# Optimization experiments

Hardware: AMD Instinct MI355X
Metric: run time of the kernel (lower is better)

## Reference

```python
import jax, jax.numpy as jnp
import numpy as np

B, S, V, D, P, HOPS = 512, 512, 50000, 300, 3, 3


def setup_inputs() -> dict:
    rng = np.random.default_rng(0)
    # left-padded text indices (zeros first, tokens last), as implied by locationed_memory
    lens = rng.integers(32, S + 1, size=B)
    txt = np.zeros((B, S), dtype=np.int64)
    for i in range(B):
        txt[i, S - lens[i]:] = rng.integers(1, V, size=lens[i])
    alens = rng.integers(1, 9, size=B)
    asp = np.zeros((B, 8), dtype=np.int64)
    for i in range(B):
        asp[i, :alens[i]] = rng.integers(1, V, size=alens[i])

    key = jax.random.key(0)
    ks = jax.random.split(key, 8)
    emb = jax.random.normal(ks[0], (V, D), dtype=jnp.float32) * 0.1
    emb = emb.at[0].set(0.0)  # padding row
    s = 1.0 / np.sqrt(D)
    Wx = jax.random.uniform(ks[1], (D, D), minval=-s, maxval=s)
    bx = jnp.zeros((D,), jnp.float32)
    Wk = jax.random.uniform(ks[2], (D, D), minval=-s, maxval=s)
    bk = jnp.zeros((D,), jnp.float32)
    Wq = jax.random.uniform(ks[3], (D, D), minval=-s, maxval=s)
    bq = jnp.zeros((D,), jnp.float32)
    w_mlp = jax.random.uniform(ks[4], (2 * D,), minval=-s, maxval=s)
    Wp = jax.random.uniform(ks[5], (D, D), minval=-s, maxval=s)
    bp = jnp.zeros((D,), jnp.float32)
    Wd = jax.random.uniform(ks[6], (P, D), minval=-s, maxval=s)
    bd = jnp.zeros((P,), jnp.float32)
    return {"text_idx": jnp.asarray(txt), "aspect_idx": jnp.asarray(asp),
            "emb": emb, "Wx": Wx, "bx": bx, "Wk": Wk, "bk": bk,
            "Wq": Wq, "bq": bq, "w_mlp": w_mlp, "Wp": Wp, "bp": bp,
            "Wd": Wd, "bd": bd}


def reference(text_idx, aspect_idx, emb, Wx, bx, Wk, bk, Wq, bq, w_mlp, Wp, bp, Wd, bd):
    lens = jnp.sum(text_idx != 0, axis=-1)                      # (B,)
    memory = emb[text_idx]                                       # (B,S,D)
    # vectorized locationed_memory: token j (0-based within the sequence) at
    # position idx = S - len + j gets weight 1 - j/len; padding positions keep 1
    pos = jnp.arange(S)[None, :]                                 # (1,S)
    j = pos - (S - lens)[:, None]                                # (B,S)
    lf = lens[:, None].astype(jnp.float32)
    w = jnp.where(j >= 0, 1.0 - j.astype(jnp.float32) / lf, 1.0)
    memory = memory * w[:, :, None]

    n_asp = jnp.sum(aspect_idx != 0, axis=-1).astype(jnp.float32)  # (B,)
    aspect = jnp.sum(emb[aspect_idx], axis=1) / n_asp[:, None]     # (B,D)

    kx = memory @ Wk.T + bk                                      # (B,S,D) key proj (same every hop)
    wk_part, wq_part = w_mlp[:D], w_mlp[D:]
    k_score = kx @ wk_part                                       # (B,S) precomputed kx contribution

    x = aspect                                                   # (B,D) == squeeze of (B,1,D)
    for _ in range(HOPS):
        x = x @ Wx.T + bx
        qx = x @ Wq.T + bq                                       # (B,D)
        # mlp score: tanh(cat(kx, qx) @ w_mlp) = tanh(kx@w_k + qx@w_q)
        score = jnp.tanh(k_score + (qx @ wq_part)[:, None])      # (B,S)
        attn = jax.nn.softmax(score, axis=-1)                    # (B,S)
        out = jnp.einsum('bs,bsd->bd', attn, kx)                 # (B,D)
        out = out @ Wp.T + bp
        x = out + x
    return x @ Wd.T + bd                                         # (B,P)
```

## Files before the change

### kernel.cpp

```cpp
#include <hip/hip_runtime.h>
#include <hip/hip_fp16.h>

#define DD 300
#define SS 512
#define VV 50000

#define CK       0
#define CQS      1
#define BU       2
#define BW1      3
#define C3A      4
#define C3B      8
#define C3C      12
#define U_OFF    16
#define UQWX_OFF 320
#define W1_OFF   640
#define W2_OFF   960
#define D0_OFF   1280
#define P1_OFF   2240
#define P2_OFF   2560
#define D1_OFF   2880
#define D2_OFF   3840
#define D3_OFF   4800
#define TAB_OFF  8192

#define FMA4(acc, s, v) { acc.x += (s)*(v).x; acc.y += (s)*(v).y; \
                          acc.z += (s)*(v).z; acc.w += (s)*(v).w; }

__device__ __forceinline__ float fast_exp_tanh(float z) {
    const float t = __expf(2.0f * z);
    return __expf(1.0f - 2.0f / (t + 1.0f));
}

__device__ __forceinline__ float wred(float v) {
    #pragma unroll
    for (int off = 32; off; off >>= 1) v += __shfl_xor(v, off);
    return v;
}

__device__ __forceinline__ void vcomb(
    const float* __restrict__ M, const float* __restrict__ sIn,
    float* __restrict__ sOut, float* __restrict__ buf,
    const int tid, const int wv, const int lane)
{
    float4 a0{0,0,0,0}, a1{0,0,0,0};
    for (int e = wv; e < DD; e += 16) {
        const float4* kr = (const float4*)(M + e * DD);
        const float s = sIn[e];
        FMA4(a0, s, kr[lane]);
        if (lane < 11) { const float4 k1 = kr[64 + lane]; FMA4(a1, s, k1); }
    }
    float4* pr = (float4*)(buf + wv * 304);
    pr[lane] = a0;
    if (lane < 11) pr[64 + lane] = a1;
    __syncthreads();
    if (tid < DD) {
        float s = 0.f;
        #pragma unroll
        for (int w = 0; w < 16; ++w) s += buf[w * 304 + tid];
        sOut[tid] = s;
    }
    __syncthreads();
}

__device__ __forceinline__ void rowcomb3(
    const float* __restrict__ M, const float (*sIn)[304], float (*sOut)[304],
    float* __restrict__ buf, const int tid, const int wv, const int lane)
{
    float4 a00{0,0,0,0}, a01{0,0,0,0}, a10{0,0,0,0},
           a11{0,0,0,0}, a20{0,0,0,0}, a21{0,0,0,0};
    for (int e = wv; e < DD; e += 16) {
        const float4* kr = (const float4*)(M + e * DD);
        const float4 k0 = kr[lane];
        const float p0 = sIn[0][e], p1 = sIn[1][e], p2 = sIn[2][e];
        FMA4(a00, p0, k0); FMA4(a10, p1, k0); FMA4(a20, p2, k0);
        if (lane < 11) {
            const float4 k1 = kr[64 + lane];
            FMA4(a01, p0, k1); FMA4(a11, p1, k1); FMA4(a21, p2, k1);
        }
    }
    float4* p0r = (float4*)(buf + (wv * 3 + 0) * 304);
    float4* p1r = (float4*)(buf + (wv * 3 + 1) * 304);
    float4* p2r = (float4*)(buf + (wv * 3 + 2) * 304);
    p0r[lane] = a00; p1r[lane] = a10; p2r[lane] = a20;
    if (lane < 11) { p0r[64+lane] = a01; p1r[64+lane] = a11; p2r[64+lane] = a21; }
    __syncthreads();
    if (tid < DD) {
        #pragma unroll
        for (int r = 0; r < 3; ++r) {
            float s = 0.f;
            for (int w = 0; w < 16; ++w) s += buf[(w * 3 + r) * 304 + tid];
            sOut[r][tid] = s;
        }
    }
    __syncthreads();
}

__device__ __forceinline__ void bpass(
    const float* __restrict__ Wp, const float* __restrict__ bp,
    const float* __restrict__ bx, const float* __restrict__ sbk,
    float* __restrict__ sB, const int wv, const int lane)
{
    const float4* b4 = (const float4*)sbk;
    const float4 k0 = b4[lane];
    const float4 k1 = (lane < 11) ? b4[64 + lane] : float4{0, 0, 0, 0};
    for (int i2 = wv; i2 < DD; i2 += 16) {
        const float4* wr = (const float4*)(Wp + i2 * DD);
        const float4 w0 = wr[lane];
        float a = w0.x * k0.x + w0.y * k0.y + w0.z * k0.z + w0.w * k0.w;
        if (lane < 11) {
            const float4 w1 = wr[64 + lane];
            a += w1.x * k1.x + w1.y * k1.y + w1.z * k1.z + w1.w * k1.w;
        }
        a = wred(a);
        if (lane == 0) sB[i2] = a + bp[i2] + bx[i2];
    }
    __syncthreads();
}

__global__ __launch_bounds__(1024) void pre(
    const float* __restrict__ Wk, const float* __restrict__ bk,
    const float* __restrict__ Wq, const float* __restrict__ bq,
    const float* __restrict__ w_mlp,
    const float* __restrict__ Wp, const float* __restrict__ bp,
    const float* __restrict__ Wx, const float* __restrict__ bx,
    const float* __restrict__ Wd, const float* __restrict__ bd,
    float* __restrict__ ws)
{
    const int blk  = blockIdx.x;
    const int tid  = threadIdx.x;
    const int wv   = tid >> 6;
    const int lane = tid & 63;
    __shared__ __align__(16) float buf[16 * 304 * 3];
    __shared__ __align__(16) float v0[304], v1[304], v2[304], v3[304], v4[304], vB[304];
    __shared__ __align__(16) float m0[3][304], m1[3][304], mW[3][304];

    if (blk == 0) {
        if (tid < DD) v0[tid] = w_mlp[tid];
        __syncthreads();
        vcomb(Wk, v0, v1, buf, tid, wv, lane);
        if (tid < DD) ws[U_OFF + tid] = v1[tid];
        if (wv == 0) {
            float c = 0.f;
            for (int j = lane; j < DD; j += 64) c += v0[j] * bk[j];
            c = wred(c);
            if (lane == 0) ws[CK] = c;
        }
        return;
    }

    if (blk == 1) {
        if (tid < DD) v0[tid] = w_mlp[DD + tid];
        __syncthreads();
        vcomb(Wq, v0, v1, buf, tid, wv, lane);
        vcomb(Wx, v1, v2, buf, tid, wv, lane);
        vcomb(Wx, v2, v3, buf, tid, wv, lane);
        vcomb(Wx, v3, v4, buf, tid, wv, lane);
        if (tid < DD) {
            ws[UQWX_OFF + tid] = v2[tid];
            ws[W1_OFF + tid]   = v3[tid];
            ws[W2_OFF + tid]   = v4[tid];
        }
        if (wv == 0) {
            float c = 0.f;
            for (int j = lane; j < DD; j += 64) c += v0[j] * bq[j] + v1[j] * bx[j];
            c = wred(c);
            if (lane == 0) ws[CQS] = c;
        }
        __syncthreads();
        if (tid < DD) v1[tid] = bk[tid];
        __syncthreads();
        bpass(Wp, bp, bx, v1, vB, wv, lane);
        if (wv == 0) {
            float a = 0.f, b = 0.f;
            for (int j = lane; j < DD; j += 64) { a += vB[j] * v2[j]; b += vB[j] * v3[j]; }
            a = wred(a); b = wred(b);
            if (lane == 0) { ws[BU] = a; ws[BW1] = b; }
        }
        return;
    }

    if (blk == 2 || blk == 3) {
        if (tid < DD) v0[tid] = w_mlp[DD + tid];
        __syncthreads();
        vcomb(Wq, v0, v1, buf, tid, wv, lane);
        vcomb(Wx, v1, v2, buf, tid, wv, lane);
        if (blk == 2) {
            vcomb(Wp, v2, v3, buf, tid, wv, lane);
            vcomb(Wk, v3, v4, buf, tid, wv, lane);
            if (tid < DD) ws[P1_OFF + tid] = v4[tid];
        } else {
            vcomb(Wx, v2, v3, buf, tid, wv, lane);
            vcomb(Wp, v3, v4, buf, tid, wv, lane);
            vcomb(Wk, v4, v0, buf, tid, wv, lane);
            if (tid < DD) ws[P2_OFF + tid] = v0[tid];
        }
        return;
    }

    for (int r = tid; r < 3 * DD; r += 1024) mW[r / DD][r % DD] = Wd[r];
    __syncthreads();

    if (blk == 4) {
        rowcomb3(Wx, mW, m0, buf, tid, wv, lane);
        rowcomb3(Wx, m0, m1, buf, tid, wv, lane);
        if (tid < DD) v1[tid] = bk[tid];
        __syncthreads();
        bpass(Wp, bp, bx, v1, vB, wv, lane);
        if (wv < 3) {
            float ca = 0.f, cb = 0.f, cc = 0.f;
            for (int j = lane; j < DD; j += 64) {
                const float b = vB[j];
                ca += m0[wv][j] * b; cb += m1[wv][j] * b; cc += mW[wv][j] * b;
            }
            ca = wred(ca); cb = wred(cb); cc = wred(cc);
            if (lane == 0) {
                ws[C3A + wv] = ca;
                ws[C3B + wv] = cb;
                ws[C3C + wv] = cc + bd[wv];
            }
        }
        rowcomb3(Wx, m1, m0, buf, tid, wv, lane);
        for (int r = tid; r < 3 * DD; r += 1024) ws[D0_OFF + r] = m0[r / DD][r % DD];
        return;
    }
    if (blk == 5) {
        rowcomb3(Wp, mW, m0, buf, tid, wv, lane);
        rowcomb3(Wk, m0, m1, buf, tid, wv, lane);
        for (int r = tid; r < 3 * DD; r += 1024) ws[D3_OFF + r] = m1[r / DD][r % DD];
        return;
    }
    if (blk == 6) {
        rowcomb3(Wx, mW, m0, buf, tid, wv, lane);
        rowcomb3(Wp, m0, m1, buf, tid, wv, lane);
        rowcomb3(Wk, m1, m0, buf, tid, wv, lane);
        for (int r = tid; r < 3 * DD; r += 1024) ws[D2_OFF + r] = m0[r / DD][r % DD];
        return;
    }
    {
        rowcomb3(Wx, mW, m0, buf, tid, wv, lane);
        rowcomb3(Wx, m0, m1, buf, tid, wv, lane);
        rowcomb3(Wp, m1, m0, buf, tid, wv, lane);
        rowcomb3(Wk, m0, m1, buf, tid, wv, lane);
        for (int r = tid; r < 3 * DD; r += 1024) ws[D1_OFF + r] = m1[r / DD][r % DD];
    }
}

__global__ __launch_bounds__(256) void build_tables(
    const float* __restrict__ emb, const float* __restrict__ wsr,
    float* __restrict__ tab)
{
    const int tid  = threadIdx.x;
    const int lane = tid & 63;
    const int m    = lane & 3;
    const int q    = lane >> 2;

    __shared__ __align__(16) float4 Vl[76 * 12];

    if (tid < 12) Vl[75 * 12 + tid] = float4{0, 0, 0, 0};
#define STAGE_V(k, off) \
    { const float4* src = (const float4*)(wsr + (off)); \
      for (int j = tid; j < 75; j += 256) Vl[j * 12 + (k)] = src[j]; }
    STAGE_V(0,  P1_OFF)
    STAGE_V(1,  P2_OFF)
    STAGE_V(2,  D1_OFF)
    STAGE_V(3,  D1_OFF + DD)
    STAGE_V(4,  D1_OFF + 2 * DD)
    STAGE_V(5,  D2_OFF)
    STAGE_V(6,  D2_OFF + DD)
    STAGE_V(7,  D2_OFF + 2 * DD)
    STAGE_V(8,  D3_OFF)
    STAGE_V(9,  D3_OFF + DD)
    STAGE_V(10, D3_OFF + 2 * DD)
    STAGE_V(11, U_OFF)
#undef STAGE_V
    __syncthreads();

    const int task = blockIdx.x * 4 + (tid >> 6);
    if (task >= VV / 16) return;
    const int row = task * 16 + q;

    const float4* er4 = (const float4*)(emb + (size_t)row * DD);

    float4 e[19];
    #pragma unroll
    for (int t = 0; t < 19; ++t) {
        const int j = m + 4 * t;
        if (j < 75) e[t] = er4[j];
        else        e[t] = float4{0, 0, 0, 0};
    }

    float acc[12];
    #pragma unroll
    for (int k = 0; k < 12; ++k) acc[k] = 0.f;

    #pragma unroll
    for (int t = 0; t < 19; ++t) {
        const int j = m + 4 * t;
        const float4* vp = &Vl[(j < 75 ? j : 75) * 12];
        const float4 ev = e[t];
        #pragma unroll
        for (int k = 0; k < 12; ++k) {
            const float4 w = vp[k];
            acc[k] += ev.x * w.x + ev.y * w.y + ev.z * w.z + ev.w * w.w;
        }
    }

    #pragma unroll
    for (int k = 0; k < 12; ++k) {
        acc[k] += __shfl_xor(acc[k], 1);
        acc[k] += __shfl_xor(acc[k], 2);
    }

    if (m == 0) {
        float4* tp = (float4*)(tab + (size_t)row * 12);
        tp[0] = float4{acc[0], acc[1], acc[2],  acc[3]};
        tp[1] = float4{acc[4], acc[5], acc[6],  acc[7]};
        tp[2] = float4{acc[8], acc[9], acc[10], acc[11]};
    }
}

__global__ __launch_bounds__(512) void k_hops(
    const int* __restrict__ text, const int* __restrict__ asp,
    const float* __restrict__ emb, float* __restrict__ out,
    const float* __restrict__ ws)
{
    const int b    = blockIdx.x;
    const int tid  = threadIdx.x;
    const int wv   = tid >> 6;
    const int lane = tid & 63;

    __shared__ __align__(16) float X0s[304];
    __shared__ float rlen[8];
    __shared__ float rp[8][6];
    __shared__ float qsv;

    const float ck  = ws[CK];
    const float cqs = ws[CQS];

    const int t = text[b * SS + tid];
    {
        const unsigned long long bal = __ballot(t != 0);
        if (lane == 0) rlen[wv] = (float)__popcll(bal);
    }
    const float4* tr = (const float4*)(ws + TAB_OFF + (size_t)t * 12);
    const float4 tA = tr[0];
    const float4 tB = tr[1];
    const float4 tC = tr[2];

    if (tid < DD) {
        float na = 0.f, a = 0.f;
        #pragma unroll
        for (int k = 0; k < 8; ++k) {
            const int idx = asp[b * 8 + k];
            na += (idx != 0) ? 1.0f : 0.0f;
            a += emb[(size_t)idx * DD + tid];
        }
        X0s[tid] = a / na;
    }
    __syncthreads();

    float lenf; int s0;
    {
        float l = 0.f;
        #pragma unroll
        for (int w = 0; w < 8; ++w) l += rlen[w];
        lenf = l; s0 = SS - (int)l;
    }
    const bool act = (tid >= s0);
    const float wg  = act ? (1.0f - (float)(tid - s0) / lenf) : 0.f;
    const float ksr = wg * tC.w + ck;

    float aw1 = 0.f, aw2 = 0.f, d12 = 0.f, o0 = 0.f, o1 = 0.f, o2 = 0.f;
    if (wv == 0) {
        float pq = 0.f, p1 = 0.f, p2 = 0.f, pd0 = 0.f, pd1 = 0.f, pd2 = 0.f;
        for (int j = lane; j < DD; j += 64) {
            const float x = X0s[j];
            pq  += x * ws[UQWX_OFF + j];
            p1  += x * ws[W1_OFF + j];
            p2  += x * ws[W2_OFF + j];
            pd0 += x * ws[D0_OFF + j];
            pd1 += x * ws[D0_OFF + DD + j];
            pd2 += x * ws[D0_OFF + 2 * DD + j];
        }
        pq = wred(pq); aw1 = wred(p1); aw2 = wred(p2);
        o0 = wred(pd0) + ws[C3A + 0] + ws[C3B + 0] + ws[C3C + 0];
        o1 = wred(pd1) + ws[C3A + 1] + ws[C3B + 1] + ws[C3C + 1];
        o2 = wred(pd2) + ws[C3A + 2] + ws[C3B + 2] + ws[C3C + 2];
        if (lane == 0) qsv = pq + cqs;
    }
    __syncthreads();

    const float bu = ws[BU], bw1 = ws[BW1];

    #pragma unroll
    for (int h = 0; h < 3; ++h) {
        const float qs = qsv;
        float p = 0.f;
        if (act) p = fast_exp_tanh(ksr + qs);
        const float pw = p * wg;
        float u0 = p, u1, u2, u3, u4 = 0.f, u5 = 0.f;
        if (h == 0)      { u1 = pw*tA.x; u2 = pw*tA.y; u3 = pw*tA.z; u4 = pw*tA.w; u5 = pw*tB.x; }
        else if (h == 1) { u1 = pw*tA.x; u2 = pw*tB.y; u3 = pw*tB.z; u4 = pw*tB.w; }
        else             { u1 = pw*tC.x; u2 = pw*tC.y; u3 = pw*tC.z; }
        u0 = wred(u0); u1 = wred(u1); u2 = wred(u2); u3 = wred(u3);
        if (h == 0) { u4 = wred(u4); u5 = wred(u5); }
        else if (h == 1) { u4 = wred(u4); }
        if (lane == 0) {
            rp[wv][0] = u0; rp[wv][1] = u1; rp[wv][2] = u2;
            rp[wv][3] = u3; rp[wv][4] = u4; rp[wv][5] = u5;
        }
        __syncthreads();
        if (wv == 0) {
            float s0_ = 0, s1_ = 0, s2_ = 0, s3_ = 0, s4_ = 0, s5_ = 0;
            #pragma unroll
            for (int w = 0; w < 8; ++w) {
                s0_ += rp[w][0]; s1_ += rp[w][1]; s2_ += rp[w][2];
                s3_ += rp[w][3]; s4_ += rp[w][4]; s5_ += rp[w][5];
            }
            const float sp  = s0_ + (float)s0 * fast_exp_tanh(ck + qs);
            const float isp = 1.0f / sp;
            if (h == 0) {
                d12 = isp * s2_;
                o0 += isp * s3_; o1 += isp * s4_; o2 += isp * s5_;
                if (lane == 0) qsv = isp * s1_ + aw1 + bu + cqs;
            } else if (h == 1) {
                o0 += isp * s2_; o1 += isp * s3_; o2 += isp * s4_;
                if (lane == 0) qsv = isp * s1_ + d12 + aw2 + bw1 + bu + cqs;
            } else if (lane == 0) {
                out[b * 3 + 0] = o0 + isp * s1_;
                out[b * 3 + 1] = o1 + isp * s2_;
                out[b * 3 + 2] = o2 + isp * s3_;
            }
        }
        if (h < 2) __syncthreads();
    }
}

extern "C" void kernel_launch(void* const* d_in, const int* in_sizes, int n_in,
                              void* d_out, int out_size, void* d_ws, size_t ws_size,
                              hipStream_t stream)
{
    const int*   text = (const int*)d_in[0];
    const int*   asp  = (const int*)d_in[1];
    const float* emb  = (const float*)d_in[2];
    const float* Wx   = (const float*)d_in[3];
    const float* bx   = (const float*)d_in[4];
    const float* Wk   = (const float*)d_in[5];
    const float* bk   = (const float*)d_in[6];
    const float* Wq   = (const float*)d_in[7];
    const float* bq   = (const float*)d_in[8];
    const float* wm   = (const float*)d_in[9];
    const float* Wp   = (const float*)d_in[10];
    const float* bp   = (const float*)d_in[11];
    const float* Wd   = (const float*)d_in[12];
    const float* bd   = (const float*)d_in[13];
    float* out = (float*)d_out;
    float* ws  = (float*)d_ws;

    pre<<<8, 1024, 0, stream>>>(Wk, bk, Wq, bq, wm, Wp, bp, Wx, bx, Wd, bd, ws);
    build_tables<<<(VV / 16 + 3) / 4, 256, 0, stream>>>(emb, ws, ws + TAB_OFF);
    k_hops<<<512, 512, 0, stream>>>(text, asp, emb, out, ws);
}
```

Before: 186.8 us.

## Parallelize weight-chain precompute across many blocks via precomputed matrix products

The serial 8-block precompute, where each block ran a long chain of dependent 300x300 matrix-vector products, is replaced by a 205-block kernel. It first forms the matrix products Wx·Wx and Wp·Wk explicitly, then runs two level kernels whose split-K blocks each handle a slice of rows and accumulate results with atomicAdd. This shortens the dependency chains and spreads the work across many compute units, which should cut the latency of the precompute stage. The cost is two extra launches, zero-initialisation of the accumulation buffers, and float atomics that make the summation order nondeterministic.

```diff
diff --git a/kernel.cpp b/kernel.cpp
--- a/kernel.cpp
+++ b/kernel.cpp
@@ -13,16 +13,22 @@
 #define C3B      8
 #define C3C      12
 #define U_OFF    16
-#define UQWX_OFF 320
-#define W1_OFF   640
-#define W2_OFF   960
-#define D0_OFF   1280
-#define P1_OFF   2240
-#define P2_OFF   2560
-#define D1_OFF   2880
-#define D2_OFF   3840
-#define D3_OFF   4800
-#define TAB_OFF  8192
+#define UQ_OFF   320
+#define UQWX_OFF 640
+#define W1_OFF   960
+#define W2_OFF   1280
+#define P1_OFF   1600
+#define P2_OFF   1920
+#define D0_OFF   2240
+#define D1_OFF   3200
+#define D2_OFF   4160
+#define D3_OFF   5120
+#define BCB_OFF  6080
+#define A1_OFF   6400
+#define A2_OFF   7360
+#define TAB_OFF  16384
+#define X2_OFF   700000
+#define C_OFF    800000
 
 #define FMA4(acc, s, v) { acc.x += (s)*(v).x; acc.y += (s)*(v).y; \
                           acc.z += (s)*(v).z; acc.w += (s)*(v).w; }
@@ -38,14 +44,14 @@
     return v;
 }
 
-__device__ __forceinline__ void vcomb(
+__device__ __forceinline__ void vcomb16(
     const float* __restrict__ M, const float* __restrict__ sIn,
     float* __restrict__ sOut, float* __restrict__ buf,
     const int tid, const int wv, const int lane)
 {
     float4 a0{0,0,0,0}, a1{0,0,0,0};
     for (int e = wv; e < DD; e += 16) {
-        const float4* kr = (const float4*)(M + e * DD);
+        const float4* kr = (const float4*)(M + (size_t)e * DD);
         const float s = sIn[e];
         FMA4(a0, s, kr[lane]);
         if (lane < 11) { const float4 k1 = kr[64 + lane]; FMA4(a1, s, k1); }
@@ -63,14 +69,14 @@
     __syncthreads();
 }
 
-__device__ __forceinline__ void rowcomb3(
+__device__ __forceinline__ void rowcomb3_16(
     const float* __restrict__ M, const float (*sIn)[304], float (*sOut)[304],
     float* __restrict__ buf, const int tid, const int wv, const int lane)
 {
     float4 a00{0,0,0,0}, a01{0,0,0,0}, a10{0,0,0,0},
            a11{0,0,0,0}, a20{0,0,0,0}, a21{0,0,0,0};
     for (int e = wv; e < DD; e += 16) {
-        const float4* kr = (const float4*)(M + e * DD);
+        const float4* kr = (const float4*)(M + (size_t)e * DD);
         const float4 k0 = kr[lane];
         const float p0 = sIn[0][e], p1 = sIn[1][e], p2 = sIn[2][e];
         FMA4(a00, p0, k0); FMA4(a10, p1, k0); FMA4(a20, p2, k0);
@@ -96,29 +102,7 @@
     __syncthreads();
 }
 
-__device__ __forceinline__ void bpass(
-    const float* __restrict__ Wp, const float* __restrict__ bp,
-    const float* __restrict__ bx, const float* __restrict__ sbk,
-    float* __restrict__ sB, const int wv, const int lane)
-{
-    const float4* b4 = (const float4*)sbk;
-    const float4 k0 = b4[lane];
-    const float4 k1 = (lane < 11) ? b4[64 + lane] : float4{0, 0, 0, 0};
-    for (int i2 = wv; i2 < DD; i2 += 16) {
-        const float4* wr = (const float4*)(Wp + i2 * DD);
-        const float4 w0 = wr[lane];
-        float a = w0.x * k0.x + w0.y * k0.y + w0.z * k0.z + w0.w * k0.w;
-        if (lane < 11) {
-            const float4 w1 = wr[64 + lane];
-            a += w1.x * k1.x + w1.y * k1.y + w1.z * k1.z + w1.w * k1.w;
-        }
-        a = wred(a);
-        if (lane == 0) sB[i2] = a + bp[i2] + bx[i2];
-    }
-    __syncthreads();
-}
-
-__global__ __launch_bounds__(1024) void pre(
+__global__ __launch_bounds__(1024) void pre1(
     const float* __restrict__ Wk, const float* __restrict__ bk,
     const float* __restrict__ Wq, const float* __restrict__ bq,
     const float* __restrict__ w_mlp,
@@ -132,117 +116,214 @@
     const int wv   = tid >> 6;
     const int lane = tid & 63;
     __shared__ __align__(16) float buf[16 * 304 * 3];
-    __shared__ __align__(16) float v0[304], v1[304], v2[304], v3[304], v4[304], vB[304];
-    __shared__ __align__(16) float m0[3][304], m1[3][304], mW[3][304];
-
-    if (blk == 0) {
+    __shared__ __align__(16) float v0[304], v1[304], vB[304];
+    __shared__ __align__(16) float m0[3][304], mW[3][304];
+    __shared__ float red[16];
+
+    if (blk < 200) {
+        const bool isC = (blk < 100);
+        const int i0 = (isC ? blk : blk - 100) * 3;
+        const float* Arows = isC ? Wp : Wx;
+        const float* Mrows = isC ? Wk : Wx;
+        const int outoff = isC ? C_OFF : X2_OFF;
+
+        for (int r = tid; r < 3 * DD; r += 1024)
+            mW[r / DD][r % DD] = Arows[i0 * DD + r];
+        __syncthreads();
+
+        float4 a00{0,0,0,0}, a01{0,0,0,0}, a10{0,0,0,0},
+               a11{0,0,0,0}, a20{0,0,0,0}, a21{0,0,0,0};
+        for (int e = wv; e < DD; e += 16) {
+            const float4* kr = (const float4*)(Mrows + (size_t)e * DD);
+            const float4 k0 = kr[lane];
+            const float p0 = mW[0][e], p1 = mW[1][e], p2 = mW[2][e];
+            FMA4(a00, p0, k0); FMA4(a10, p1, k0); FMA4(a20, p2, k0);
+            if (lane < 11) {
+                const float4 k1 = kr[64 + lane];
+                FMA4(a01, p0, k1); FMA4(a11, p1, k1); FMA4(a21, p2, k1);
+            }
+        }
+        float4* p0r = (float4*)(buf + (wv * 3 + 0) * 304);
+        float4* p1r = (float4*)(buf + (wv * 3 + 1) * 304);
+        float4* p2r = (float4*)(buf + (wv * 3 + 2) * 304);
+        p0r[lane] = a00; p1r[lane] = a10; p2r[lane] = a20;
+        if (lane < 11) { p0r[64+lane] = a01; p1r[64+lane] = a11; p2r[64+lane] = a21; }
+        __syncthreads();
+        if (tid < DD) {
+            #pragma unroll
+            for (int r = 0; r < 3; ++r) {
+                float s = 0.f;
+                for (int w = 0; w < 16; ++w) s += buf[(w * 3 + r) * 304 + tid];
+                ws[outoff + (size_t)(i0 + r) * DD + tid] = s;
+            }
+        }
+        return;
+    }
+
+    if (blk == 200) {
         if (tid < DD) v0[tid] = w_mlp[tid];
         __syncthreads();
-        vcomb(Wk, v0, v1, buf, tid, wv, lane);
+        vcomb16(Wk, v0, v1, buf, tid, wv, lane);
         if (tid < DD) ws[U_OFF + tid] = v1[tid];
-        if (wv == 0) {
-            float c = 0.f;
-            for (int j = lane; j < DD; j += 64) c += v0[j] * bk[j];
-            c = wred(c);
-            if (lane == 0) ws[CK] = c;
+        float p = (tid < DD) ? v0[tid] * bk[tid] : 0.f;
+        p = wred(p);
+        if (lane == 0) red[wv] = p;
+        __syncthreads();
+        if (tid == 0) {
+            float s = 0.f;
+            for (int w = 0; w < 16; ++w) s += red[w];
+            ws[CK] = s;
         }
         return;
     }
 
-    if (blk == 1) {
+    if (blk == 201) {
         if (tid < DD) v0[tid] = w_mlp[DD + tid];
         __syncthreads();
-        vcomb(Wq, v0, v1, buf, tid, wv, lane);
-        vcomb(Wx, v1, v2, buf, tid, wv, lane);
-        vcomb(Wx, v2, v3, buf, tid, wv, lane);
-        vcomb(Wx, v3, v4, buf, tid, wv, lane);
-        if (tid < DD) {
-            ws[UQWX_OFF + tid] = v2[tid];
-            ws[W1_OFF + tid]   = v3[tid];
-            ws[W2_OFF + tid]   = v4[tid];
-        }
-        if (wv == 0) {
-            float c = 0.f;
-            for (int j = lane; j < DD; j += 64) c += v0[j] * bq[j] + v1[j] * bx[j];
-            c = wred(c);
-            if (lane == 0) ws[CQS] = c;
-        }
-        __syncthreads();
-        if (tid < DD) v1[tid] = bk[tid];
-        __syncthreads();
-        bpass(Wp, bp, bx, v1, vB, wv, lane);
-        if (wv == 0) {
-            float a = 0.f, b = 0.f;
-            for (int j = lane; j < DD; j += 64) { a += vB[j] * v2[j]; b += vB[j] * v3[j]; }
-            a = wred(a); b = wred(b);
-            if (lane == 0) { ws[BU] = a; ws[BW1] = b; }
+        vcomb16(Wq, v0, v1, buf, tid, wv, lane);
+        if (tid < DD) ws[UQ_OFF + tid] = v1[tid];
+        float p = (tid < DD) ? (v0[tid] * bq[tid] + v1[tid] * bx[tid]) : 0.f;
+        p = wred(p);
+        if (lane == 0) red[wv] = p;
+        __syncthreads();
+        if (tid == 0) {
+            float s = 0.f;
+            for (int w = 0; w < 16; ++w) s += red[w];
+            ws[CQS] = s;
         }
         return;
     }
 
-    if (blk == 2 || blk == 3) {
-        if (tid < DD) v0[tid] = w_mlp[DD + tid];
-        __syncthreads();
-        vcomb(Wq, v0, v1, buf, tid, wv, lane);
-        vcomb(Wx, v1, v2, buf, tid, wv, lane);
-        if (blk == 2) {
-            vcomb(Wp, v2, v3, buf, tid, wv, lane);
-            vcomb(Wk, v3, v4, buf, tid, wv, lane);
-            if (tid < DD) ws[P1_OFF + tid] = v4[tid];
+    if (blk == 202) {
+        if (tid < DD) v0[tid] = bk[tid];
+        __syncthreads();
+        {
+            const float4* b4 = (const float4*)v0;
+            const float4 k0 = b4[lane];
+            const float4 k1 = (lane < 11) ? b4[64 + lane] : float4{0, 0, 0, 0};
+            for (int i2 = wv; i2 < DD; i2 += 16) {
+                const float4* wr = (const float4*)(Wp + (size_t)i2 * DD);
+                const float4 w0 = wr[lane];
+                float a = w0.x * k0.x + w0.y * k0.y + w0.z * k0.z + w0.w * k0.w;
+                if (lane < 11) {
+                    const float4 w1 = wr[64 + lane];
+                    a += w1.x * k1.x + w1.y * k1.y + w1.z * k1.z + w1.w * k1.w;
+                }
+                a = wred(a);
+                if (lane == 0) { vB[i2] = a + bp[i2] + bx[i2]; }
+            }
+        }
+        __syncthreads();
+        if (tid < DD) ws[BCB_OFF + tid] = vB[tid];
+        if (wv < 3) {
+            float a = 0.f;
+            for (int j = lane; j < DD; j += 64) a += Wd[wv * DD + j] * vB[j];
+            a = wred(a);
+            if (lane == 0) ws[C3C + wv] = a + bd[wv];
+        }
+        return;
+    }
+
+    if (blk == 203) {
+        for (int r = tid; r < 3 * DD; r += 1024) mW[r / DD][r % DD] = Wd[r];
+        __syncthreads();
+        rowcomb3_16(Wx, mW, m0, buf, tid, wv, lane);
+        for (int r = tid; r < 3 * DD; r += 1024)
+            ws[A1_OFF + (r / DD) * DD + (r % DD)] = m0[r / DD][r % DD];
+        return;
+    }
+
+    {
+#define ZZ(off, len) for (int j = tid; j < (len); j += 1024) ws[(off) + j] = 0.f;
+        ZZ(UQWX_OFF, 300) ZZ(W1_OFF, 300) ZZ(W2_OFF, 300)
+        ZZ(P1_OFF, 300)   ZZ(P2_OFF, 300)
+        ZZ(A2_OFF, 900)   ZZ(D0_OFF, 900) ZZ(D1_OFF, 900)
+        ZZ(D2_OFF, 900)   ZZ(D3_OFF, 900)
+#undef ZZ
+    }
+}
+
+__global__ __launch_bounds__(256) void plvl(
+    const float* __restrict__ Wx, const float* __restrict__ Wd,
+    float* __restrict__ ws, const int lvl)
+{
+    const int S2[11] = {UQ_OFF, UQ_OFF, -1, -2, -3, -1, -2, -3,
+                        A1_OFF, A1_OFF + 300, A1_OFF + 600};
+    const int M2[11] = {0, 1, 1, 1, 1, 2, 2, 2, 2, 2, 2};
+    const int T2[11] = {UQWX_OFF, W1_OFF, A2_OFF, A2_OFF + 300, A2_OFF + 600,
+                        D3_OFF, D3_OFF + 300, D3_OFF + 600,
+                        D2_OFF, D2_OFF + 300, D2_OFF + 600};
+    const int S3[9]  = {UQWX_OFF, UQWX_OFF, W1_OFF,
+                        A2_OFF, A2_OFF + 300, A2_OFF + 600,
+                        A2_OFF, A2_OFF + 300, A2_OFF + 600};
+    const int M3[9]  = {1, 2, 2, 2, 2, 2, 0, 0, 0};
+    const int T3[9]  = {W2_OFF, P1_OFF, P2_OFF,
+                        D1_OFF, D1_OFF + 300, D1_OFF + 600,
+                        D0_OFF, D0_OFF + 300, D0_OFF + 600};
+    const int nt = (lvl == 2) ? 11 : 9;
+
+    const int tid  = threadIdx.x;
+    const int lane = tid & 63;
+    const int wv   = tid >> 6;
+    const int bi   = blockIdx.x;
+
+    __shared__ __align__(16) float sv[304];
+    __shared__ __align__(16) float buf[4 * 304];
+
+    if (bi >= nt * 16) {
+        if (lvl == 2) {
+            if (wv < 3) {
+                float a = 0.f;
+                for (int j = lane; j < DD; j += 64)
+                    a += ws[A1_OFF + wv * DD + j] * ws[BCB_OFF + j];
+                a = wred(a);
+                if (lane == 0) ws[C3A + wv] = a;
+            }
         } else {
-            vcomb(Wx, v2, v3, buf, tid, wv, lane);
-            vcomb(Wp, v3, v4, buf, tid, wv, lane);
-            vcomb(Wk, v4, v0, buf, tid, wv, lane);
-            if (tid < DD) ws[P2_OFF + tid] = v0[tid];
+            for (int job = wv; job < 5; job += 4) {
+                const int so = (job == 0) ? UQWX_OFF
+                             : (job == 1) ? W1_OFF
+                             : A2_OFF + (job - 2) * DD;
+                float a = 0.f;
+                for (int j = lane; j < DD; j += 64)
+                    a += ws[so + j] * ws[BCB_OFF + j];
+                a = wred(a);
+                if (lane == 0) {
+                    if (job == 0)      ws[BU]  = a;
+                    else if (job == 1) ws[BW1] = a;
+                    else               ws[C3B + job - 2] = a;
+                }
+            }
         }
         return;
     }
 
-    for (int r = tid; r < 3 * DD; r += 1024) mW[r / DD][r % DD] = Wd[r];
-    __syncthreads();
-
-    if (blk == 4) {
-        rowcomb3(Wx, mW, m0, buf, tid, wv, lane);
-        rowcomb3(Wx, m0, m1, buf, tid, wv, lane);
-        if (tid < DD) v1[tid] = bk[tid];
-        __syncthreads();
-        bpass(Wp, bp, bx, v1, vB, wv, lane);
-        if (wv < 3) {
-            float ca = 0.f, cb = 0.f, cc = 0.f;
-            for (int j = lane; j < DD; j += 64) {
-                const float b = vB[j];
-                ca += m0[wv][j] * b; cb += m1[wv][j] * b; cc += mW[wv][j] * b;
-            }
-            ca = wred(ca); cb = wred(cb); cc = wred(cc);
-            if (lane == 0) {
-                ws[C3A + wv] = ca;
-                ws[C3B + wv] = cb;
-                ws[C3C + wv] = cc + bd[wv];
-            }
-        }
-        rowcomb3(Wx, m1, m0, buf, tid, wv, lane);
-        for (int r = tid; r < 3 * DD; r += 1024) ws[D0_OFF + r] = m0[r / DD][r % DD];
-        return;
-    }
-    if (blk == 5) {
-        rowcomb3(Wp, mW, m0, buf, tid, wv, lane);
-        rowcomb3(Wk, m0, m1, buf, tid, wv, lane);
-        for (int r = tid; r < 3 * DD; r += 1024) ws[D3_OFF + r] = m1[r / DD][r % DD];
-        return;
-    }
-    if (blk == 6) {
-        rowcomb3(Wx, mW, m0, buf, tid, wv, lane);
-        rowcomb3(Wp, m0, m1, buf, tid, wv, lane);
-        rowcomb3(Wk, m1, m0, buf, tid, wv, lane);
-        for (int r = tid; r < 3 * DD; r += 1024) ws[D2_OFF + r] = m0[r / DD][r % DD];
-        return;
-    }
-    {
-        rowcomb3(Wx, mW, m0, buf, tid, wv, lane);
-        rowcomb3(Wx, m0, m1, buf, tid, wv, lane);
-        rowcomb3(Wp, m1, m0, buf, tid, wv, lane);
-        rowcomb3(Wk, m0, m1, buf, tid, wv, lane);
-        for (int r = tid; r < 3 * DD; r += 1024) ws[D1_OFF + r] = m1[r / DD][r % DD];
+    const int t = bi >> 4, g = bi & 15;
+    const int sc = (lvl == 2) ? S2[t] : S3[t];
+    const int mt = (lvl == 2) ? M2[t] : M3[t];
+    const int dofs = (lvl == 2) ? T2[t] : T3[t];
+    const float* M = (mt == 0) ? Wx : (mt == 1) ? (ws + X2_OFF) : (ws + C_OFF);
+
+    for (int j = tid; j < 304; j += 256)
+        sv[j] = (j < DD) ? ((sc >= 0) ? ws[sc + j] : Wd[(-sc - 1) * DD + j]) : 0.f;
+    __syncthreads();
+
+    const bool lo = (lane < 11);
+    float4 a0{0,0,0,0}, a1{0,0,0,0};
+    const int e0 = g * 19, e1 = min(e0 + 19, DD);
+    for (int e = e0 + wv; e < e1; e += 4) {
+        const float4* kr = (const float4*)(M + (size_t)e * DD);
+        const float s = sv[e];
+        FMA4(a0, s, kr[lane]);
+        if (lo) { const float4 k1 = kr[64 + lane]; FMA4(a1, s, k1); }
+    }
+    float4* pr = (float4*)(buf + wv * 304);
+    pr[lane] = a0;
+    if (lo) pr[64 + lane] = a1;
+    __syncthreads();
+    for (int j = tid; j < DD; j += 256) {
+        const float s = buf[j] + buf[304 + j] + buf[608 + j] + buf[912 + j];
+        atomicAdd(ws + dofs + j, s);
     }
 }
 
@@ -458,7 +539,9 @@
     float* out = (float*)d_out;
     float* ws  = (float*)d_ws;
 
-    pre<<<8, 1024, 0, stream>>>(Wk, bk, Wq, bq, wm, Wp, bp, Wx, bx, Wd, bd, ws);
+    pre1<<<205, 1024, 0, stream>>>(Wk, bk, Wq, bq, wm, Wp, bp, Wx, bx, Wd, bd, ws);
+    plvl<<<11 * 16 + 1, 256, 0, stream>>>(Wx, Wd, ws, 2);
+    plvl<<<9 * 16 + 1, 256, 0, stream>>>(Wx, Wd, ws, 3);
     build_tables<<<(VV / 16 + 3) / 4, 256, 0, stream>>>(emb, ws, ws + TAB_OFF);
     k_hops<<<512, 512, 0, stream>>>(text, asp, emb, out, ws);
 }
```

Result: faster. 173.6 us (-7.1%).
